# Performance work log

Measured on AMD Instinct MI355X. Metric: run time of the kernel, lower is better.

## Reference

```python
import jax, jax.numpy as jnp
import numpy as np


def _prelu(v, a):
    return jnp.where(v >= 0, v, a * v)


def setup_inputs() -> dict:
    key = jax.random.key(0)
    B, H, L, N, DC = 16, 64, 16384, 32, 128
    ks = jax.random.split(key, 10)
    x = jax.random.normal(ks[0], (B, H, L), jnp.float32)
    cond = jax.random.normal(ks[1], (B, DC), jnp.float32)
    # input pointwise linear (applied over channel dim)
    linear_w = jax.random.normal(ks[2], (H, H), jnp.float32) / np.sqrt(H)
    linear_b = jnp.zeros((H,), jnp.float32)
    prelu1_a = jnp.float32(0.25)
    # S4D parameters (S4D-Lin init): A = -exp(log_A_real) + i*A_imag
    log_dt = jax.random.uniform(ks[3], (H,), jnp.float32,
                                minval=float(np.log(1e-3)), maxval=float(np.log(1e-1)))
    log_A_real = jnp.log(0.5 * jnp.ones((H, N), jnp.float32))
    A_imag = jnp.tile(np.pi * jnp.arange(N, dtype=np.float32), (H, 1))
    C_re = 0.5 * jax.random.normal(ks[4], (H, N), jnp.float32)
    C_im = 0.5 * jax.random.normal(ks[5], (H, N), jnp.float32)
    Dskip = jax.random.normal(ks[6], (H,), jnp.float32)
    # S4 output position-wise linear
    out_w = jax.random.normal(ks[7], (H, H), jnp.float32) / np.sqrt(H)
    out_b = jnp.zeros((H,), jnp.float32)
    # FiLM: cond -> (gamma, beta)
    film_w = jax.random.normal(ks[8], (2 * H, DC), jnp.float32) / np.sqrt(DC)
    film_b = jnp.zeros((2 * H,), jnp.float32)
    prelu2_a = jnp.float32(0.25)
    # depthwise 1x1 conv residual: one scalar per channel
    res_w = jax.random.normal(ks[9], (H,), jnp.float32) / np.sqrt(H)
    return dict(x=x, cond=cond, linear_w=linear_w, linear_b=linear_b,
                prelu1_a=prelu1_a, log_dt=log_dt, log_A_real=log_A_real,
                A_imag=A_imag, C_re=C_re, C_im=C_im, Dskip=Dskip,
                out_w=out_w, out_b=out_b, film_w=film_w, film_b=film_b,
                prelu2_a=prelu2_a, res_w=res_w)


def reference(x, cond, linear_w, linear_b, prelu1_a, log_dt, log_A_real,
              A_imag, C_re, C_im, Dskip, out_w, out_b, film_w, film_b,
              prelu2_a, res_w):
    B, H, L = x.shape
    # linear over channel dim (B H L -> B L H -> linear -> B H L)
    h = jnp.einsum('gh,bhl->bgl', linear_w, x) + linear_b[None, :, None]
    h = _prelu(h, prelu1_a)
    # ---- S4D kernel generation (ZOH discretization) ----
    dt = jnp.exp(log_dt)                       # (H,)
    A = -jnp.exp(log_A_real) + 1j * A_imag     # (H, N) complex
    dtA = A * dt[:, None]                      # (H, N)
    Cd = (C_re + 1j * C_im) * (jnp.exp(dtA) - 1.0) / A
    vand = jnp.exp(dtA[:, :, None] * jnp.arange(L, dtype=jnp.float32))  # (H,N,L)
    K = 2.0 * jnp.einsum('hn,hnl->hl', Cd, vand).real  # (H, L)
    # ---- FFT convolution (causal, linear conv via 2L-point FFT) ----
    n = 2 * L
    y = jnp.fft.irfft(jnp.fft.rfft(h, n=n) * jnp.fft.rfft(K, n=n), n=n)[..., :L]
    y = y + h * Dskip[None, :, None]
    # S4 output position-wise linear
    y = jnp.einsum('gh,bhl->bgl', out_w, y) + out_b[None, :, None]
    # BatchNorm1d(affine=False), training-mode batch statistics
    mean = jnp.mean(y, axis=(0, 2), keepdims=True)
    var = jnp.var(y, axis=(0, 2), keepdims=True)
    y = (y - mean) / jnp.sqrt(var + 1e-5)
    # FiLM conditioning
    gb = cond @ film_w.T + film_b              # (B, 2H)
    gamma, beta = jnp.split(gb, 2, axis=-1)
    y = gamma[:, :, None] * y + beta[:, :, None]
    y = _prelu(y, prelu2_a)
    # depthwise 1x1 conv residual
    return y + res_w[None, :, None] * x
```

## Files before the change

kernel.cpp:

```cpp
#include <hip/hip_runtime.h>
#include <math.h>

#define BB 16
#define HH 64
#define LL 16384
#define NST 32
#define LC 256
#define CC 64
#define BL (BB*LL)

typedef _Float16 f16;
typedef f16  f16x8 __attribute__((ext_vector_type(8)));
typedef float f32x4 __attribute__((ext_vector_type(4)));

#define OFF_H   ((size_t)0)
#define OFF_P   ((size_t)8388608)
#define OFF_S   ((size_t)12582912)
#define OFF_T   ((size_t)14680064)
#define OFF_V   ((size_t)16777216)
#define OFF_U   ((size_t)17301504)
#define OFF_PW  ((size_t)17825792)
#define OFF_WL  ((size_t)17833984)
#define OFF_GB  ((size_t)17838080)
#define OFF_BN  ((size_t)17840128)
#define OFF_BNF ((size_t)17840256)

__global__ void k0_setup(const float* __restrict__ log_dt,
                         const float* __restrict__ log_A_real,
                         const float* __restrict__ A_imag,
                         const float* __restrict__ C_re,
                         const float* __restrict__ C_im,
                         const float* __restrict__ cond,
                         const float* __restrict__ film_w,
                         const float* __restrict__ film_b,
                         float* __restrict__ ws) {
    int t = threadIdx.x, bid = blockIdx.x;
    if (bid < 8) {
        float4* pw = (float4*)(ws + OFF_PW);
        float2* wl = (float2*)(ws + OFF_WL);
        int idx = bid * 256 + t;
        int ch = idx >> 5;
        float dt  = expf(log_dt[ch]);
        float are = -expf(log_A_real[idx]);
        float aim = A_imag[idx];
        float dr = are * dt, di = aim * dt;
        float er = expf(dr);
        float wr = er * cosf(di);
        float wi = er * sinf(di);
        float inv = 1.0f / (are * are + aim * aim);
        float gr = ((wr - 1.0f) * are + wi * aim) * inv;
        float gi = (wi * are - (wr - 1.0f) * aim) * inv;
        float cr = C_re[idx], ci = C_im[idx];
        float cdr = cr * gr - ci * gi;
        float cdi = cr * gi + ci * gr;
        pw[idx] = make_float4(wr, wi, 2.0f * cdr, 2.0f * cdi);
        float erL = expf(dr * (float)LC);
        wl[idx] = make_float2(erL * cosf(di * (float)LC), erL * sinf(di * (float)LC));
    } else {
        float* gb = ws + OFF_GB;
        int o = (bid - 8) * 256 + t;
        int b = o >> 7, j = o & 127;
        float acc = film_b[j];
        for (int q = 0; q < 128; q++)
            acc = fmaf(cond[b * 128 + q], film_w[j * 128 + q], acc);
        gb[o] = acc;
    }
}

__global__ __launch_bounds__(256) void kprep(const float* __restrict__ log_dt,
                                             const float* __restrict__ log_A,
                                             const float* __restrict__ A_imag,
                                             const float* __restrict__ Dskip,
                                             float* __restrict__ ws) {
    __shared__ float drs[32], dis[32], c2r[32], c2i[32];
    int ch = blockIdx.x, t = threadIdx.x;
    if (t < 32) {
        float dt = expf(log_dt[ch]);
        float are = -expf(log_A[ch * 32 + t]);
        float aim = A_imag[ch * 32 + t];
        drs[t] = are * dt; dis[t] = aim * dt;
        float4 p = ((const float4*)(ws + OFF_PW))[ch * 32 + t];
        c2r[t] = p.z; c2i[t] = p.w;
    }
    __syncthreads();
    float acc = 0.0f;
    float fd = (float)t;
    for (int n = 0; n < 32; n++) {
        float e = expf(drs[n] * fd);
        float ph = dis[n] * fd;
        acc += c2r[n] * e * cosf(ph) - c2i[n] * e * sinf(ph);
    }
    if (t == 0) acc += Dskip[ch];
    ws[OFF_P + (size_t)ch * 256 + t] = acc;
}

__global__ __launch_bounds__(256) void kbuild(const float* __restrict__ log_dt,
                                              const float* __restrict__ log_A,
                                              const float* __restrict__ A_imag,
                                              float* __restrict__ ws) {
    __shared__ float Kl[256];
    __shared__ float drs[32], dis[32], c2r[32], c2i[32];
    int bid = blockIdx.x;
    int ch = bid >> 4, part = bid & 15;
    int t = threadIdx.x;
    if (t < 32) {
        float dt = expf(log_dt[ch]);
        float are = -expf(log_A[ch * 32 + t]);
        float aim = A_imag[ch * 32 + t];
        drs[t] = are * dt; dis[t] = aim * dt;
        float4 p = ((const float4*)(ws + OFF_PW))[ch * 32 + t];
        c2r[t] = p.z; c2i[t] = p.w;
    }
    Kl[t] = ws[OFF_P + (size_t)ch * 256 + t];
    __syncthreads();
    f16* T = (f16*)(ws + OFF_T) + (size_t)ch * 65536;
    {
        int r0 = part * 16;
#pragma unroll
        for (int i = 0; i < 2; i++) {
            int idx = t + i * 256;
            int row = r0 + (idx >> 5);
            int c0 = (idx & 31) * 8;
            f16 vals[8];
#pragma unroll
            for (int j = 0; j < 8; j++) {
                int c = c0 + j;
                vals[j] = (f16)((c <= row) ? Kl[row - c] : 0.0f);
            }
            *(float4*)(T + (size_t)row * 256 + c0) = *(const float4*)vals;
        }
    }
    if (part < 8) {
        f16* V = (f16*)(ws + OFF_V) + (size_t)ch * 16384;
        int row = part * 8 + (t >> 5);
        int c0 = (t & 31) * 8;
        int n = row & 31;
        f16 vals[8];
#pragma unroll
        for (int j = 0; j < 8; j++) {
            float fe = (float)(255 - (c0 + j));
            float e = expf(drs[n] * fe);
            float ph = dis[n] * fe;
            vals[j] = (f16)((row < 32) ? e * cosf(ph) : e * sinf(ph));
        }
        *(float4*)(V + (size_t)row * 256 + c0) = *(const float4*)vals;
    } else {
        f16* U = (f16*)(ws + OFF_U) + (size_t)ch * 16384;
        int l = (part - 8) * 32 + (t >> 3);
        int c0 = (t & 7) * 8;
        float fl1 = (float)(l + 1);
        f16 vals[8];
#pragma unroll
        for (int nn = 0; nn < 4; nn++) {
            int n = (c0 >> 1) + nn;
            float e = expf(drs[n] * fl1);
            float ph = dis[n] * fl1;
            float wre = e * cosf(ph), wim = e * sinf(ph);
            float re = c2r[n] * wre - c2i[n] * wim;
            float im = c2r[n] * wim + c2i[n] * wre;
            vals[2 * nn]     = (f16)re;
            vals[2 * nn + 1] = (f16)(-im);
        }
        *(float4*)(U + (size_t)l * 64 + c0) = *(const float4*)vals;
    }
}

__global__ __launch_bounds__(256) void k_cm1m(const float* __restrict__ x,
                                              const float* __restrict__ W,
                                              const float* __restrict__ bias,
                                              f16* __restrict__ dst,
                                              const float* __restrict__ aptr) {
    int t = threadIdx.x, bi = blockIdx.x;
    int b = bi >> 6;
    int wv = t >> 6, lane = t & 63;
    int qd = lane >> 4, ln = lane & 15;
    int colw = ((bi & 63) << 8) + wv * 64;
    const float* xb = x + (size_t)b * HH * LL;
    f32x4 acc[4][4];
#pragma unroll
    for (int a = 0; a < 4; a++)
#pragma unroll
        for (int nb = 0; nb < 4; nb++) acc[a][nb] = (f32x4)0.0f;
#pragma unroll
    for (int ks = 0; ks < 2; ks++) {
        f16x8 whi[4], wlo[4];
#pragma unroll
        for (int a = 0; a < 4; a++) {
            const float* wp = W + (size_t)(a * 16 + ln) * 64 + ks * 32 + qd * 8;
#pragma unroll
            for (int j = 0; j < 8; j++) {
                float f = wp[j];
                f16 hv = (f16)f;
                whi[a][j] = hv;
                wlo[a][j] = (f16)(f - (float)hv);
            }
        }
        f16x8 bhi[4], blo[4];
#pragma unroll
        for (int nb = 0; nb < 4; nb++) {
            const float* xp = xb + (size_t)(ks * 32 + qd * 8) * LL + colw + nb * 16 + ln;
#pragma unroll
            for (int j = 0; j < 8; j++) {
                float f = xp[(size_t)j * LL];
                f16 hv = (f16)f;
                bhi[nb][j] = hv;
                blo[nb][j] = (f16)(f - (float)hv);
            }
        }
#pragma unroll
        for (int a = 0; a < 4; a++)
#pragma unroll
            for (int nb = 0; nb < 4; nb++)
                acc[a][nb] = __builtin_amdgcn_mfma_f32_16x16x32_f16(whi[a], bhi[nb], acc[a][nb], 0, 0, 0);
#pragma unroll
        for (int a = 0; a < 4; a++)
#pragma unroll
            for (int nb = 0; nb < 4; nb++)
                acc[a][nb] = __builtin_amdgcn_mfma_f32_16x16x32_f16(whi[a], blo[nb], acc[a][nb], 0, 0, 0);
#pragma unroll
        for (int a = 0; a < 4; a++)
#pragma unroll
            for (int nb = 0; nb < 4; nb++)
                acc[a][nb] = __builtin_amdgcn_mfma_f32_16x16x32_f16(wlo[a], bhi[nb], acc[a][nb], 0, 0, 0);
    }
    float a1 = *aptr;
    f16* dp = dst + (size_t)b * HH * LL;
#pragma unroll
    for (int a = 0; a < 4; a++)
#pragma unroll
        for (int r = 0; r < 4; r++) {
            int g = a * 16 + qd * 4 + r;
            float bb = bias[g];
            f16* gp = dp + (size_t)g * LL + colw + ln;
#pragma unroll
            for (int nb = 0; nb < 4; nb++) {
                float v = acc[a][nb][r] + bb;
                v = (v >= 0.0f) ? v : a1 * v;
                gp[nb * 16] = (f16)v;
            }
        }
}

__global__ __launch_bounds__(256) void k_cm2m(const f16* __restrict__ y1,
                                              const float* __restrict__ W,
                                              const float* __restrict__ bias,
                                              float* __restrict__ dst,
                                              float* __restrict__ ws) {
    __shared__ float bns[64], bnss[64];
    int t = threadIdx.x, bi = blockIdx.x;
    int b = bi >> 6;
    int wv = t >> 6, lane = t & 63;
    int qd = lane >> 4, ln = lane & 15;
    int colw = ((bi & 63) << 8) + wv * 64;
    const f16* yb = y1 + (size_t)b * HH * LL;
    if (t < 64) { bns[t] = 0.0f; bnss[t] = 0.0f; }
    __syncthreads();
    f32x4 acc[4][4];
#pragma unroll
    for (int a = 0; a < 4; a++)
#pragma unroll
        for (int nb = 0; nb < 4; nb++) acc[a][nb] = (f32x4)0.0f;
#pragma unroll
    for (int ks = 0; ks < 2; ks++) {
        f16x8 whi[4], wlo[4];
#pragma unroll
        for (int a = 0; a < 4; a++) {
            const float* wp = W + (size_t)(a * 16 + ln) * 64 + ks * 32 + qd * 8;
#pragma unroll
            for (int j = 0; j < 8; j++) {
                float f = wp[j];
                f16 hv = (f16)f;
                whi[a][j] = hv;
                wlo[a][j] = (f16)(f - (float)hv);
            }
        }
        f16x8 bf[4];
#pragma unroll
        for (int nb = 0; nb < 4; nb++) {
            const f16* yp = yb + (size_t)(ks * 32 + qd * 8) * LL + colw + nb * 16 + ln;
#pragma unroll
            for (int j = 0; j < 8; j++)
                bf[nb][j] = yp[(size_t)j * LL];
        }
#pragma unroll
        for (int a = 0; a < 4; a++)
#pragma unroll
            for (int nb = 0; nb < 4; nb++)
                acc[a][nb] = __builtin_amdgcn_mfma_f32_16x16x32_f16(whi[a], bf[nb], acc[a][nb], 0, 0, 0);
#pragma unroll
        for (int a = 0; a < 4; a++)
#pragma unroll
            for (int nb = 0; nb < 4; nb++)
                acc[a][nb] = __builtin_amdgcn_mfma_f32_16x16x32_f16(wlo[a], bf[nb], acc[a][nb], 0, 0, 0);
    }
    float* dp = dst + (size_t)b * HH * LL;
#pragma unroll
    for (int a = 0; a < 4; a++)
#pragma unroll
        for (int r = 0; r < 4; r++) {
            int g = a * 16 + qd * 4 + r;
            float bb = bias[g];
            float* gp = dp + (size_t)g * LL + colw + ln;
            float s = 0.0f, ssq = 0.0f;
#pragma unroll
            for (int nb = 0; nb < 4; nb++) {
                float v = acc[a][nb][r] + bb;
                gp[nb * 16] = v;
                s += v; ssq += v * v;
            }
#pragma unroll
            for (int off = 1; off < 16; off <<= 1) {
                s += __shfl_xor(s, off);
                ssq += __shfl_xor(ssq, off);
            }
            if (ln == 0) {
                atomicAdd(&bns[g], s);
                atomicAdd(&bnss[g], ssq);
            }
        }
    __syncthreads();
    if (t < 64) {
        float* part = ws + OFF_P;
        part[(size_t)bi * 128 + t] = bns[t];
        part[(size_t)bi * 128 + 64 + t] = bnss[t];
    }
}

__global__ __launch_bounds__(256) void gemmA(float* __restrict__ ws) {
    __shared__ __align__(16) char smem[25600];
    f16* Vs = (f16*)smem;
    f16* Hs = (f16*)(smem + 5120);
    int t = threadIdx.x;
    int bid = blockIdx.x;
    int ch = bid & 63, ntile = bid >> 6;
    const f16* Vm = (const f16*)(ws + OFF_V) + (size_t)ch * 16384;
    const f16* H  = (const f16*)(ws + OFF_H);
    int w = t >> 6, lane = t & 63;
    int qd = lane >> 4, ln = lane & 15;
    f32x4 acc[4][4];
#pragma unroll
    for (int a = 0; a < 4; a++)
#pragma unroll
        for (int nb = 0; nb < 4; nb++) acc[a][nb] = (f32x4)0.0f;
    int colg = ntile * 256 + t;
    const f16* hcol = H + ((size_t)(colg >> 6) * 64 + ch) * 16384 + (size_t)(colg & 63) * 256;
    int vrow = t >> 2, vkg = t & 3;
    for (int k0 = 0; k0 < 256; k0 += 32) {
        __syncthreads();
        *(float4*)&Vs[vrow * 40 + vkg * 8] = *(const float4*)(Vm + vrow * 256 + k0 + vkg * 8);
#pragma unroll
        for (int kg = 0; kg < 4; kg++)
            *(float4*)&Hs[t * 40 + kg * 8] = *(const float4*)(hcol + k0 + kg * 8);
        __syncthreads();
        f16x8 af[4], bf[4];
#pragma unroll
        for (int a = 0; a < 4; a++) af[a] = *(f16x8*)&Vs[(a * 16 + ln) * 40 + qd * 8];
#pragma unroll
        for (int nb = 0; nb < 4; nb++) bf[nb] = *(f16x8*)&Hs[(w * 64 + nb * 16 + ln) * 40 + qd * 8];
#pragma unroll
        for (int a = 0; a < 4; a++)
#pragma unroll
            for (int nb = 0; nb < 4; nb++)
                acc[a][nb] = __builtin_amdgcn_mfma_f32_16x16x32_f16(af[a], bf[nb], acc[a][nb], 0, 0, 0);
    }
    float* P = ws + OFF_P;
#pragma unroll
    for (int a = 0; a < 4; a++)
#pragma unroll
        for (int nb = 0; nb < 4; nb++)
#pragma unroll
            for (int r = 0; r < 4; r++) {
                int row = a * 16 + qd * 4 + r;
                int col = ntile * 256 + w * 64 + nb * 16 + ln;
                P[((size_t)ch * 64 + row) * 1024 + col] = acc[a][nb][r];
            }
}

__global__ __launch_bounds__(256) void k3_scan(float* __restrict__ ws) {
    int tid = blockIdx.x * 256 + threadIdx.x;
    int ch = tid >> 9, b = (tid >> 5) & 15, n = tid & 31;
    const float* P = ws + OFF_P;
    f16* S = (f16*)(ws + OFF_S);
    float2 wl = ((const float2*)(ws + OFF_WL))[ch * 32 + n];
    float sr = 0.0f, si = 0.0f;
    const float* pre = P + ((size_t)ch * 64 + n) * 1024 + b * 64;
    const float* pim = P + ((size_t)ch * 64 + 32 + n) * 1024 + b * 64;
    f16* srow = S + ((size_t)ch * 1024 + b * 64) * 64 + 2 * n;
    for (int c = 0; c < 64; c++) {
        srow[c * 64]     = (f16)sr;
        srow[c * 64 + 1] = (f16)si;
        float pr = pre[c], pi = pim[c];
        float nr = fmaf(wl.x, sr, fmaf(-wl.y, si, pr));
        float ni = fmaf(wl.y, sr, fmaf(wl.x, si, pi));
        sr = nr; si = ni;
    }
}

__global__ __launch_bounds__(256) void gemmMain(float* __restrict__ ws) {
    __shared__ __align__(16) f16 Ys[64 * 136];
    int t = threadIdx.x;
    int bid = blockIdx.x;
    int ch = bid & 63, ntile = bid >> 6;
    const f16* Tm = (const f16*)(ws + OFF_T) + (size_t)ch * 65536;
    const f16* Um = (const f16*)(ws + OFF_U) + (size_t)ch * 16384;
    const f16* H  = (const f16*)(ws + OFF_H);
    const f16* St = (const f16*)(ws + OFF_S);
    f16* y1 = (f16*)(ws + OFF_H);
    int w = t >> 6, lane = t & 63;
    int qd = lane >> 4, ln = lane & 15;
    int rowbase = w * 64;
    f32x4 acc[4][4];
#pragma unroll
    for (int a = 0; a < 4; a++)
#pragma unroll
        for (int nb = 0; nb < 4; nb++) acc[a][nb] = (f32x4)0.0f;
    const f16* hcolp[4];
    const f16* scolp[4];
#pragma unroll
    for (int nb = 0; nb < 4; nb++) {
        int colg = ntile * 64 + nb * 16 + ln;
        hcolp[nb] = H + ((size_t)(colg >> 6) * 64 + ch) * 16384 + (size_t)(colg & 63) * 256;
        scolp[nb] = St + ((size_t)ch * 1024 + colg) * 64;
    }
    for (int k0 = 0; k0 < 256; k0 += 32) {
        if (k0 <= rowbase + 63) {
            f16x8 bf[4];
#pragma unroll
            for (int nb = 0; nb < 4; nb++)
                bf[nb] = *(const f16x8*)(hcolp[nb] + k0 + qd * 8);
#pragma unroll
            for (int a = 0; a < 4; a++) {
                if (k0 <= rowbase + a * 16 + 15) {
                    f16x8 af = *(const f16x8*)(Tm + (size_t)(rowbase + a * 16 + ln) * 256 + k0 + qd * 8);
#pragma unroll
                    for (int nb = 0; nb < 4; nb++)
                        acc[a][nb] = __builtin_amdgcn_mfma_f32_16x16x32_f16(af, bf[nb], acc[a][nb], 0, 0, 0);
                }
            }
        }
    }
#pragma unroll
    for (int k0 = 0; k0 < 64; k0 += 32) {
        f16x8 bf[4];
#pragma unroll
        for (int nb = 0; nb < 4; nb++)
            bf[nb] = *(const f16x8*)(scolp[nb] + k0 + qd * 8);
#pragma unroll
        for (int a = 0; a < 4; a++) {
            f16x8 af = *(const f16x8*)(Um + (size_t)(rowbase + a * 16 + ln) * 64 + k0 + qd * 8);
#pragma unroll
            for (int nb = 0; nb < 4; nb++)
                acc[a][nb] = __builtin_amdgcn_mfma_f32_16x16x32_f16(af, bf[nb], acc[a][nb], 0, 0, 0);
        }
    }
    int ocol = t >> 2, ojg = t & 3;
    int ocolg = ntile * 64 + ocol;
    f16* ybase = y1 + ((size_t)(ocolg >> 6) * 64 + ch) * 16384 + (size_t)(ocolg & 63) * 256;
    for (int hf = 0; hf < 2; hf++) {
        __syncthreads();
        if ((w >> 1) == hf) {
            int jl0 = (w & 1) * 64;
#pragma unroll
            for (int a = 0; a < 4; a++)
#pragma unroll
                for (int nb = 0; nb < 4; nb++)
#pragma unroll
                    for (int r = 0; r < 4; r++)
                        Ys[(nb * 16 + ln) * 136 + jl0 + a * 16 + qd * 4 + r] = (f16)acc[a][nb][r];
        }
        __syncthreads();
#pragma unroll
        for (int i = 0; i < 4; i++)
            *(float4*)(ybase + hf * 128 + ojg * 32 + i * 8) =
                *(const float4*)&Ys[ocol * 136 + ojg * 32 + i * 8];
    }
}

__global__ __launch_bounds__(256) void k5c_bnfin(float* __restrict__ ws) {
    int ch = blockIdx.x;
    int t = threadIdx.x;
    const float* part = ws + OFF_P;
    float s = 0.0f, ss = 0.0f;
#pragma unroll
    for (int i = 0; i < 4; i++) {
        int pb = t + i * 256;
        s  += part[(size_t)pb * 128 + ch];
        ss += part[(size_t)pb * 128 + 64 + ch];
    }
    for (int off = 32; off; off >>= 1) {
        s += __shfl_xor(s, off);
        ss += __shfl_xor(ss, off);
    }
    __shared__ float as_[4], ass_[4];
    int wv = t >> 6;
    if ((t & 63) == 0) { as_[wv] = s; ass_[wv] = ss; }
    __syncthreads();
    if (t == 0) {
        float S = as_[0] + as_[1] + as_[2] + as_[3];
        float SS = ass_[0] + ass_[1] + ass_[2] + ass_[3];
        float cnt = (float)BL;
        float mean = S / cnt;
        float var = SS / cnt - mean * mean;
        ws[OFF_BNF + ch] = mean;
        ws[OFF_BNF + 64 + ch] = 1.0f / sqrtf(var + 1e-5f);
    }
}

__global__ __launch_bounds__(256) void k6_final(const float* __restrict__ x,
                                                const float* __restrict__ ws,
                                                const float* __restrict__ a2p,
                                                const float* __restrict__ res_w,
                                                float* __restrict__ out) {
    int bi = blockIdx.x;
    int t = threadIdx.x;
    int row = bi >> 4;
    int b = row >> 6, ch = row & 63;
    float gamma = ws[OFF_GB + b * 128 + ch];
    float beta  = ws[OFF_GB + b * 128 + 64 + ch];
    float mean = ws[OFF_BNF + ch];
    float inv  = ws[OFF_BNF + 64 + ch];
    float scale = gamma * inv;
    float shift = beta - scale * mean;
    float rw = res_w[ch];
    float a2 = *a2p;
    size_t i4 = (size_t)row * (LL / 4) + (size_t)(bi & 15) * 256 + t;
    float4 y = ((const float4*)out)[i4];
    float4 xv = ((const float4*)x)[i4];
    float v;
    v = fmaf(scale, y.x, shift); v = (v >= 0.0f) ? v : a2 * v; y.x = fmaf(rw, xv.x, v);
    v = fmaf(scale, y.y, shift); v = (v >= 0.0f) ? v : a2 * v; y.y = fmaf(rw, xv.y, v);
    v = fmaf(scale, y.z, shift); v = (v >= 0.0f) ? v : a2 * v; y.z = fmaf(rw, xv.z, v);
    v = fmaf(scale, y.w, shift); v = (v >= 0.0f) ? v : a2 * v; y.w = fmaf(rw, xv.w, v);
    ((float4*)out)[i4] = y;
}

extern "C" void kernel_launch(void* const* d_in, const int* in_sizes, int n_in,
                              void* d_out, int out_size, void* d_ws, size_t ws_size,
                              hipStream_t stream) {
    const float* x        = (const float*)d_in[0];
    const float* cond     = (const float*)d_in[1];
    const float* linear_w = (const float*)d_in[2];
    const float* linear_b = (const float*)d_in[3];
    const float* prelu1_a = (const float*)d_in[4];
    const float* log_dt   = (const float*)d_in[5];
    const float* log_A    = (const float*)d_in[6];
    const float* A_imag   = (const float*)d_in[7];
    const float* C_re     = (const float*)d_in[8];
    const float* C_im     = (const float*)d_in[9];
    const float* Dskip    = (const float*)d_in[10];
    const float* out_w    = (const float*)d_in[11];
    const float* out_b    = (const float*)d_in[12];
    const float* film_w   = (const float*)d_in[13];
    const float* film_b   = (const float*)d_in[14];
    const float* prelu2_a = (const float*)d_in[15];
    const float* res_w    = (const float*)d_in[16];
    float* ws  = (float*)d_ws;
    float* out = (float*)d_out;
    f16* hbuf = (f16*)(ws + OFF_H);
    f16* y1   = (f16*)(ws + OFF_H);

    hipLaunchKernelGGL(k0_setup, dim3(16), dim3(256), 0, stream,
                       log_dt, log_A, A_imag, C_re, C_im, cond, film_w, film_b, ws);
    hipLaunchKernelGGL(kprep, dim3(64), dim3(256), 0, stream,
                       log_dt, log_A, A_imag, Dskip, ws);
    hipLaunchKernelGGL(kbuild, dim3(1024), dim3(256), 0, stream,
                       log_dt, log_A, A_imag, ws);
    hipLaunchKernelGGL(k_cm1m, dim3(1024), dim3(256), 0, stream,
                       x, linear_w, linear_b, hbuf, prelu1_a);
    hipLaunchKernelGGL(gemmA, dim3(256), dim3(256), 0, stream, ws);
    hipLaunchKernelGGL(k3_scan, dim3(128), dim3(256), 0, stream, ws);
    hipLaunchKernelGGL(gemmMain, dim3(1024), dim3(256), 0, stream, ws);
    hipLaunchKernelGGL(k_cm2m, dim3(1024), dim3(256), 0, stream,
                       y1, out_w, out_b, out, ws);
    hipLaunchKernelGGL(k5c_bnfin, dim3(64), dim3(256), 0, stream, ws);
    hipLaunchKernelGGL(k6_final, dim3(16384), dim3(256), 0, stream,
                       x, ws, prelu2_a, res_w, out);
}
```

Measured before the change: 291.5 us.

## Stage T/U and H/S tiles through LDS in gemmMain instead of direct global loads

Each K-step of the main GEMM now loads the Toeplitz-block A tile (T or U) and the B tile (H or S) cooperatively into padded shared memory, then reads MFMA operands from LDS. Before, every wave read its fragments straight from global memory with strided 16-byte loads. The change is meant to coalesce those loads and cut redundant global traffic. It adds two barriers per K-step with no double buffering, and the LDS footprint grows, which may reduce occupancy.

```diff
diff --git a/kernel.cpp b/kernel.cpp
--- a/kernel.cpp
+++ b/kernel.cpp
@@ -397,7 +397,10 @@
 }
 
 __global__ __launch_bounds__(256) void gemmMain(float* __restrict__ ws) {
-    __shared__ __align__(16) f16 Ys[64 * 136];
+    __shared__ __align__(16) char smem[25600];
+    f16* Ts = (f16*)smem;
+    f16* Hs = (f16*)(smem + 20480);
+    f16* Ys = (f16*)smem;
     int t = threadIdx.x;
     int bid = blockIdx.x;
     int ch = bid & 63, ntile = bid >> 6;
@@ -408,30 +411,32 @@
     f16* y1 = (f16*)(ws + OFF_H);
     int w = t >> 6, lane = t & 63;
     int qd = lane >> 4, ln = lane & 15;
-    int rowbase = w * 64;
     f32x4 acc[4][4];
 #pragma unroll
     for (int a = 0; a < 4; a++)
 #pragma unroll
         for (int nb = 0; nb < 4; nb++) acc[a][nb] = (f32x4)0.0f;
-    const f16* hcolp[4];
-    const f16* scolp[4];
-#pragma unroll
-    for (int nb = 0; nb < 4; nb++) {
-        int colg = ntile * 64 + nb * 16 + ln;
-        hcolp[nb] = H + ((size_t)(colg >> 6) * 64 + ch) * 16384 + (size_t)(colg & 63) * 256;
-        scolp[nb] = St + ((size_t)ch * 1024 + colg) * 64;
-    }
+    int scol = t >> 2, skg = t & 3;
+    int colg = ntile * 64 + scol;
+    const f16* hcol = H + ((size_t)(colg >> 6) * 64 + ch) * 16384 + (size_t)(colg & 63) * 256;
+    const f16* sscol = St + ((size_t)ch * 1024 + colg) * 64;
     for (int k0 = 0; k0 < 256; k0 += 32) {
-        if (k0 <= rowbase + 63) {
+        __syncthreads();
+        if (t >= k0 - 16) {
+#pragma unroll
+            for (int kg = 0; kg < 4; kg++)
+                *(float4*)&Ts[t * 40 + kg * 8] = *(const float4*)(Tm + t * 256 + k0 + kg * 8);
+        }
+        *(float4*)&Hs[scol * 40 + skg * 8] = *(const float4*)(hcol + k0 + skg * 8);
+        __syncthreads();
+        if (k0 <= w * 64 + 63) {
             f16x8 bf[4];
 #pragma unroll
-            for (int nb = 0; nb < 4; nb++)
-                bf[nb] = *(const f16x8*)(hcolp[nb] + k0 + qd * 8);
+            for (int nb = 0; nb < 4; nb++) bf[nb] = *(f16x8*)&Hs[(nb * 16 + ln) * 40 + qd * 8];
 #pragma unroll
             for (int a = 0; a < 4; a++) {
-                if (k0 <= rowbase + a * 16 + 15) {
-                    f16x8 af = *(const f16x8*)(Tm + (size_t)(rowbase + a * 16 + ln) * 256 + k0 + qd * 8);
+                if (k0 <= w * 64 + a * 16 + 15) {
+                    f16x8 af = *(f16x8*)&Ts[(w * 64 + a * 16 + ln) * 40 + qd * 8];
 #pragma unroll
                     for (int nb = 0; nb < 4; nb++)
                         acc[a][nb] = __builtin_amdgcn_mfma_f32_16x16x32_f16(af, bf[nb], acc[a][nb], 0, 0, 0);
@@ -439,15 +444,19 @@
             }
         }
     }
-#pragma unroll
     for (int k0 = 0; k0 < 64; k0 += 32) {
+        __syncthreads();
+#pragma unroll
+        for (int kg = 0; kg < 4; kg++)
+            *(float4*)&Ts[t * 40 + kg * 8] = *(const float4*)(Um + t * 64 + k0 + kg * 8);
+        *(float4*)&Hs[scol * 40 + skg * 8] = *(const float4*)(sscol + k0 + skg * 8);
+        __syncthreads();
         f16x8 bf[4];
 #pragma unroll
-        for (int nb = 0; nb < 4; nb++)
-            bf[nb] = *(const f16x8*)(scolp[nb] + k0 + qd * 8);
+        for (int nb = 0; nb < 4; nb++) bf[nb] = *(f16x8*)&Hs[(nb * 16 + ln) * 40 + qd * 8];
 #pragma unroll
         for (int a = 0; a < 4; a++) {
-            f16x8 af = *(const f16x8*)(Um + (size_t)(rowbase + a * 16 + ln) * 64 + k0 + qd * 8);
+            f16x8 af = *(f16x8*)&Ts[(w * 64 + a * 16 + ln) * 40 + qd * 8];
 #pragma unroll
             for (int nb = 0; nb < 4; nb++)
                 acc[a][nb] = __builtin_amdgcn_mfma_f32_16x16x32_f16(af, bf[nb], acc[a][nb], 0, 0, 0);
```

Measured after the change: 288.3 us. Within noise of the previous version (-1.1%).
